# Kernel tuning notes

Measured on AMD Instinct MI355X. Metric: run time of the kernel, lower is better.

Reference implementation:

```python
import jax, jax.numpy as jnp
import numpy as np

NUM_STATES = 8
HIDDEN_DIM = 1024
BATCH = 16384
DT = 0.01
PLANCK = 1.0
EPS_NORM = 1e-8
EPS_LOG = 1e-12


def setup_inputs() -> dict:
    key = jax.random.key(0)
    k1, k2, k3, k4, k5 = jax.random.split(key, 5)
    inv_sqrt_d = 1.0 / np.sqrt(HIDDEN_DIM)
    return {
        "input_state": jax.random.normal(k1, (BATCH, HIDDEN_DIM), dtype=jnp.float32),
        "amplitude_real": jax.random.normal(k2, (NUM_STATES, HIDDEN_DIM), dtype=jnp.float32) * inv_sqrt_d,
        "amplitude_imag": jax.random.normal(k3, (NUM_STATES, HIDDEN_DIM), dtype=jnp.float32) * inv_sqrt_d,
        "hamiltonian": jax.random.normal(k4, (NUM_STATES, NUM_STATES), dtype=jnp.float32) * 0.01,
        "projections": jax.random.normal(k5, (NUM_STATES, HIDDEN_DIM, HIDDEN_DIM), dtype=jnp.float32) * 0.01,
    }


def reference(input_state, amplitude_real, amplitude_imag, hamiltonian, projections):
    # complex amplitudes, normalized per state over hidden dim
    amps = amplitude_real + 1j * amplitude_imag  # [S, D] complex64
    norms = jnp.sum(jnp.abs(amps) ** 2, axis=1, keepdims=True)
    amps = amps / jnp.sqrt(norms + EPS_NORM)

    # unitary Hamiltonian evolution: expm(-i H dt / hbar) on the tiny SxS matrix
    H = (hamiltonian + hamiltonian.T) * 0.5
    U = jax.scipy.linalg.expm((-1j * DT / PLANCK) * H.astype(jnp.complex64))  # [S, S]
    amps = U @ amps  # [S, D]

    # decoherence at time_step=0: factor exp(0)=1, thermal noise scale 0 -> identity

    # superposed output: out[b,e] = sum_s Re(amps[s,e]) * (x @ P_s)[b,e]
    w = jnp.real(amps)  # [S, D]
    proj = jnp.einsum('bd,sde->bse', input_state, projections)  # [B, S, D]
    measured_output = jnp.einsum('bse,se->be', proj, w)  # [B, D]

    # measurement probabilities (computational basis)
    probs = jnp.abs(amps) ** 2
    probs = probs / (probs.sum(axis=0, keepdims=True) + EPS_NORM)
    collapse_prob = probs.mean(axis=1)  # [S]

    # metrics on rank-1 density matrix rho = outer(v, conj(v)), v = amps.flatten():
    # eigenvalues are {||v||^2, 0, ...} so the von Neumann entropy reduces to one term,
    # and sum|rho| = (sum|v|)^2, tr|diag| = sum|v|^2.
    v_abs = jnp.abs(amps.reshape(-1))
    lam = jnp.sum(v_abs ** 2)
    entanglement_entropy = -(lam * jnp.log(lam + EPS_LOG))
    coherence = jnp.sum(v_abs) ** 2 - lam

    amplitude_distribution = jnp.abs(amps) ** 2
    phase_evolution = jnp.angle(amps)

    return (measured_output, collapse_prob, entanglement_entropy, coherence,
            amplitude_distribution, phase_evolution)
```

## Files before the change

### kernel.cpp

```cpp
#include <hip/hip_runtime.h>
#include <hip/hip_bf16.h>

#define NSTATES 8
#define HD      1024
#define NBATCH  16384
#define NT      16

#define OUT_MEAS 0
#define OUT_CP   16777216
#define OUT_ENT  16777224
#define OUT_COH  16777225
#define OUT_AD   16777226
#define OUT_PH   16785418

typedef __attribute__((ext_vector_type(8))) short short8;
typedef __attribute__((ext_vector_type(4))) float f32x4;

__device__ __forceinline__ short f2bf(float f) {
    union { float f; unsigned u; } x; x.f = f;
    unsigned r = x.u + 0x7fffu + ((x.u >> 16) & 1u);
    return (short)(r >> 16);
}

__device__ __forceinline__ unsigned cvtpk(float lo, float hi) {
    unsigned r;
    asm("v_cvt_pk_bf16_f32 %0, %1, %2" : "=v"(r) : "v"(lo), "v"(hi));
    return r;
}

__device__ __forceinline__ short8 pack8pk(float4 a, float4 b) {
    union { unsigned u[4]; short8 s; } r;
    r.u[0] = cvtpk(a.x, a.y);
    r.u[1] = cvtpk(a.z, a.w);
    r.u[2] = cvtpk(b.x, b.y);
    r.u[3] = cvtpk(b.z, b.w);
    return r.s;
}

__global__ __launch_bounds__(1024) void k_amps(const float* __restrict__ AR,
                                               const float* __restrict__ AI,
                                               const float* __restrict__ H,
                                               float* __restrict__ out,
                                               float* __restrict__ w) {
    __shared__ float redA[16 * NSTATES];
    __shared__ float redB[16 * 10];
    __shared__ float norms[NSTATES];
    __shared__ float sA[8][8], sA2[8][8], sA3[8][8];
    __shared__ float Ur[8][8], Ui[8][8];
    __shared__ float lamsa[2];

    const int tid = threadIdx.x;
    const int lane = tid & 63, wid = tid >> 6;
    const int d = tid;

    float arv[NSTATES], aiv[NSTATES];
    #pragma unroll
    for (int s = 0; s < NSTATES; s++) {
        arv[s] = AR[s * HD + d];
        aiv[s] = AI[s * HD + d];
    }
    float p[NSTATES];
    #pragma unroll
    for (int s = 0; s < NSTATES; s++) p[s] = arv[s] * arv[s] + aiv[s] * aiv[s];
    #pragma unroll
    for (int s = 0; s < NSTATES; s++)
        #pragma unroll
        for (int o = 32; o > 0; o >>= 1) p[s] += __shfl_down(p[s], o, 64);
    if (lane == 0)
        #pragma unroll
        for (int s = 0; s < NSTATES; s++) redA[wid * NSTATES + s] = p[s];
    if (tid < 64) {
        int i = tid >> 3, j = tid & 7;
        sA[i][j] = 0.5f * (H[i * 8 + j] + H[j * 8 + i]) * 0.01f;
    }
    __syncthreads();
    if (tid < 8) {
        float acc = 0.f;
        #pragma unroll
        for (int v = 0; v < 16; v++) acc += redA[v * NSTATES + tid];
        norms[tid] = acc;
    }
    if (tid < 64) {
        int i = tid >> 3, j = tid & 7;
        float acc = 0.f;
        #pragma unroll
        for (int k = 0; k < 8; k++) acc += sA[i][k] * sA[k][j];
        sA2[i][j] = acc;
    }
    __syncthreads();
    if (tid < 64) {
        int i = tid >> 3, j = tid & 7;
        float acc = 0.f;
        #pragma unroll
        for (int k = 0; k < 8; k++) acc += sA2[i][k] * sA[k][j];
        sA3[i][j] = acc;
        Ur[i][j] = ((i == j) ? 1.f : 0.f) - 0.5f * sA2[i][j];
        Ui[i][j] = -(sA[i][j] - sA3[i][j] * (1.f / 6.f));
    }
    __syncthreads();

    #pragma unroll
    for (int s = 0; s < NSTATES; s++) {
        float inv = 1.0f / sqrtf(norms[s] + 1e-8f);
        arv[s] *= inv;
        aiv[s] *= inv;
    }
    float nr[NSTATES], ni[NSTATES];
    #pragma unroll
    for (int s = 0; s < NSTATES; s++) {
        float xr = 0.f, xi = 0.f;
        #pragma unroll
        for (int t = 0; t < NSTATES; t++) {
            float ur = Ur[s][t], ui = Ui[s][t];
            xr += ur * arv[t] - ui * aiv[t];
            xi += ur * aiv[t] + ui * arv[t];
        }
        nr[s] = xr; ni[s] = xi;
    }
    float dist[NSTATES], csum = 0.f, sabs = 0.f;
    #pragma unroll
    for (int s = 0; s < NSTATES; s++) {
        dist[s] = nr[s] * nr[s] + ni[s] * ni[s];
        csum += dist[s];
        sabs += sqrtf(dist[s]);
    }
    #pragma unroll
    for (int s = 0; s < NSTATES; s++) {
        out[OUT_AD + s * HD + d] = dist[s];
        out[OUT_PH + s * HD + d] = atan2f(ni[s], nr[s]);
        w[s * HD + d] = nr[s];
    }
    float cinv = 1.0f / (csum + 1e-8f);
    float q[10];
    #pragma unroll
    for (int s = 0; s < NSTATES; s++) q[s] = dist[s] * cinv;
    q[8] = csum; q[9] = sabs;
    #pragma unroll
    for (int v = 0; v < 10; v++)
        #pragma unroll
        for (int o = 32; o > 0; o >>= 1) q[v] += __shfl_down(q[v], o, 64);
    if (lane == 0)
        #pragma unroll
        for (int v = 0; v < 10; v++) redB[wid * 10 + v] = q[v];
    __syncthreads();
    if (tid < 10) {
        float acc = 0.f;
        #pragma unroll
        for (int v = 0; v < 16; v++) acc += redB[v * 10 + tid];
        if (tid < 8)       out[OUT_CP + tid] = acc * (1.0f / HD);
        else               lamsa[tid - 8] = acc;
    }
    __syncthreads();
    if (tid == 0) {
        float lam = lamsa[0], sa = lamsa[1];
        out[OUT_ENT] = -(lam * logf(lam + 1e-12f));
        out[OUT_COH] = sa * sa - lam;
    }
}

__global__ __launch_bounds__(256) void k_project_t(const float* __restrict__ P,
                                                   const float* __restrict__ w,
                                                   short* __restrict__ Mt) {
    __shared__ float tile[64][65];
    int d0 = (blockIdx.x >> 4) * 64;
    int e0 = (blockIdx.x & 15) * 64;
    int tx = threadIdx.x & 63, ty = threadIdx.x >> 6;
    float wv[NSTATES];
    #pragma unroll
    for (int s = 0; s < NSTATES; s++) wv[s] = w[s * HD + e0 + tx];
    #pragma unroll
    for (int j = 0; j < 16; j++) {
        int r = ty + 4 * j;
        float acc = 0.f;
        #pragma unroll
        for (int s = 0; s < NSTATES; s++)
            acc += wv[s] * P[(size_t)s * HD * HD + (size_t)(d0 + r) * HD + e0 + tx];
        tile[r][tx] = acc;
    }
    __syncthreads();
    #pragma unroll
    for (int j = 0; j < 16; j++) {
        int er = ty + 4 * j;
        Mt[(size_t)(e0 + er) * HD + d0 + tx] = f2bf(tile[tx][er]);
    }
}


__device__ __forceinline__ void stage_half_B(const short* __restrict__ srcBase,
                                             int rowbase, int h, int t2,
                                             short* dst, const int* goff,
                                             const int* ldsoff) {
    #pragma unroll
    for (int i = 0; i < 2; i++) {
        const short* g = srcBase + (size_t)(rowbase + h * 128) * HD + t2 * 64 + goff[i];
        __builtin_amdgcn_global_load_lds(
            (const __attribute__((address_space(1))) void*)g,
            (__attribute__((address_space(3))) void*)(dst + h * 8192 + ldsoff[i]),
            16, 0, 0);
    }
}

#define XLOAD(dst, h, t2)                                                      \
    {                                                                          \
        const float* b_ = X + (size_t)(brow + (h) * 128) * HD + (t2) * 64;     \
        dst[0] = *reinterpret_cast<const float4*>(b_ + goff[0]);               \
        dst[1] = *reinterpret_cast<const float4*>(b_ + goff[0] + 4);           \
        dst[2] = *reinterpret_cast<const float4*>(b_ + goff[1]);               \
        dst[3] = *reinterpret_cast<const float4*>(b_ + goff[1] + 4);           \
    }

#define XWRITE(dstlds, src)                                                    \
    {                                                                          \
        *reinterpret_cast<short8*>((dstlds) + ldsoff[0]) = pack8pk(src[0], src[1]); \
        *reinterpret_cast<short8*>((dstlds) + ldsoff[1]) = pack8pk(src[2], src[3]); \
    }

#define LOAD_A(qa)                                                             \
    _Pragma("unroll") for (int mf = 0; mf < 4; mf++)                           \
    _Pragma("unroll") for (int kk = 0; kk < 2; kk++)                           \
        af[mf][kk] = *reinterpret_cast<const short8*>(                         \
            &Acur[((qa) * 128 + wr64 + mf * 16 + ln15) * 64 + kx[kk]]);

#define LOAD_B_TO(dst, qb)                                                     \
    _Pragma("unroll") for (int nf = 0; nf < 2; nf++)                           \
    _Pragma("unroll") for (int kk = 0; kk < 2; kk++)                           \
        dst[nf][kk] = *reinterpret_cast<const short8*>(                        \
            &Bcur[((qb) * 128 + wn32 + nf * 16 + ln15) * 64 + kx[kk]]);

#define MFMA_P(qa, qb, breg)                                                   \
    _Pragma("unroll") for (int mf = 0; mf < 4; mf++)                           \
    _Pragma("unroll") for (int nf = 0; nf < 2; nf++)                           \
    _Pragma("unroll") for (int kk = 0; kk < 2; kk++)                           \
        acc[(qa) * 4 + mf][(qb) * 2 + nf] =                                    \
            __builtin_amdgcn_mfma_f32_16x16x32_bf16(                           \
                af[mf][kk], breg[nf][kk], acc[(qa) * 4 + mf][(qb) * 2 + nf], 0, 0, 0);

#define STORE_Q(qa, qb)                                                        \
    _Pragma("unroll") for (int mf = 0; mf < 4; mf++)                           \
    _Pragma("unroll") for (int nf = 0; nf < 2; nf++)                           \
    _Pragma("unroll") for (int j = 0; j < 4; j++) {                            \
        int r = brow + (qa) * 128 + wr64 + mf * 16 + l16 * 4 + j;              \
        int c = bcol + (qb) * 128 + wn32 + nf * 16 + ln15;                     \
        out[(size_t)r * HD + c] = acc[(qa) * 4 + mf][(qb) * 2 + nf][j];        \
    }

__global__ __launch_bounds__(512, 1) void k_gemm_jit3(const float* __restrict__ X,
                                                      const short* __restrict__ Mt,
                                                      float* __restrict__ out) {
    __shared__ short As[2][256 * 64];
    __shared__ short Bs[2][256 * 64];

    const int bid = blockIdx.x;
    const int swz = (bid & 7) * 32 + (bid >> 3);
    const int brow = (swz >> 2) * 256;
    const int bcol = (swz & 3) * 256;

    const int tid  = threadIdx.x;
    const int lane = tid & 63, wid = tid >> 6;
    const int wr = wid >> 2, wn = wid & 3;
    const int ln15 = lane & 15, l16 = lane >> 4;
    const int wr64 = wr * 64;
    const int wn32 = wn * 32;

    int kx[2];
    kx[0] = ((l16 + 0) ^ (ln15 & 7)) * 8;
    kx[1] = ((l16 + 4) ^ (ln15 & 7)) * 8;

    int goff[2], ldsoff[2];
    #pragma unroll
    for (int i = 0; i < 2; i++) {
        int c = tid + 512 * i;
        int row = c >> 3, kc = c & 7;
        goff[i]   = row * HD + ((kc ^ (row & 7)) * 8);
        ldsoff[i] = c * 8;
    }

    short* A0 = &As[0][0]; short* A1b = &As[1][0];
    short* B0 = &Bs[0][0]; short* B1b = &Bs[1][0];

    f32x4 acc[8][4];
    #pragma unroll
    for (int m = 0; m < 8; m++)
        #pragma unroll
        for (int n = 0; n < 4; n++) acc[m][n] = (f32x4){0.f, 0.f, 0.f, 0.f};

    float4 xrL[4], xrH[4];

    XLOAD(xrL, 0, 0);
    XLOAD(xrH, 1, 0);
    stage_half_B(Mt, bcol, 0, 0, B0, goff, ldsoff);
    stage_half_B(Mt, bcol, 1, 0, B0, goff, ldsoff);
    stage_half_B(Mt, bcol, 1, 1, B1b, goff, ldsoff);
    XWRITE(A0, xrL);
    XWRITE(A0 + 8192, xrH);
    XLOAD(xrL, 0, 1);
    asm volatile("s_waitcnt vmcnt(6) lgkmcnt(0)" ::: "memory");
    __builtin_amdgcn_s_barrier();

    short8 af[4][2], bfL[2][2], bfH[2][2];

    #pragma unroll 1
    for (int t = 0; t < NT - 1; t++) {
        const int cur = t & 1;
        short* Acur  = cur ? A1b : A0;
        short* Bcur  = cur ? B1b : B0;
        short* Anext = cur ? A0 : A1b;
        short* Bnext = cur ? B0 : B1b;

        LOAD_A(0); LOAD_B_TO(bfL, 0);
        if (t + 1 < NT) XLOAD(xrH, 1, (t + 1));
        __builtin_amdgcn_s_barrier();
        __builtin_amdgcn_s_setprio(1);
        MFMA_P(0, 0, bfL);
        __builtin_amdgcn_s_setprio(0);

        LOAD_B_TO(bfH, 1);
        if (t + 1 < NT) stage_half_B(Mt, bcol, 0, t + 1, Bnext, goff, ldsoff);
        __builtin_amdgcn_s_barrier();
        __builtin_amdgcn_s_setprio(1);
        MFMA_P(0, 1, bfH);
        __builtin_amdgcn_s_setprio(0);

        LOAD_A(1);
        if (t + 1 < NT) XWRITE(Anext, xrL);
        __builtin_amdgcn_s_barrier();
        __builtin_amdgcn_s_setprio(1);
        MFMA_P(1, 1, bfH);
        __builtin_amdgcn_s_setprio(0);

        if (t + 1 < NT) XWRITE(Anext + 8192, xrH);
        if (t + 2 < NT) {
            XLOAD(xrL, 0, (t + 2));
            stage_half_B(Mt, bcol, 1, t + 2, Bcur, goff, ldsoff);
        }
        if (t + 2 < NT)      asm volatile("s_waitcnt vmcnt(6) lgkmcnt(0)" ::: "memory");
        else if (t + 1 < NT) asm volatile("s_waitcnt vmcnt(0) lgkmcnt(0)" ::: "memory");
        __builtin_amdgcn_s_barrier();
        __builtin_amdgcn_s_setprio(1);
        MFMA_P(1, 0, bfL);
        __builtin_amdgcn_s_setprio(0);
    }

    {
        short* Acur = A1b;
        short* Bcur = B1b;

        LOAD_A(0); LOAD_B_TO(bfL, 0);
        __builtin_amdgcn_s_setprio(1);
        MFMA_P(0, 0, bfL);
        __builtin_amdgcn_s_setprio(0);
        STORE_Q(0, 0);

        LOAD_B_TO(bfH, 1);
        __builtin_amdgcn_s_setprio(1);
        MFMA_P(0, 1, bfH);
        __builtin_amdgcn_s_setprio(0);
        STORE_Q(0, 1);

        LOAD_A(1);
        __builtin_amdgcn_s_setprio(1);
        MFMA_P(1, 1, bfH);
        __builtin_amdgcn_s_setprio(0);
        STORE_Q(1, 1);

        __builtin_amdgcn_s_setprio(1);
        MFMA_P(1, 0, bfL);
        __builtin_amdgcn_s_setprio(0);
        STORE_Q(1, 0);
    }
}

extern "C" void kernel_launch(void* const* d_in, const int* in_sizes, int n_in,
                              void* d_out, int out_size, void* d_ws, size_t ws_size,
                              hipStream_t stream) {
    const float* X  = (const float*)d_in[0];
    const float* AR = (const float*)d_in[1];
    const float* AI = (const float*)d_in[2];
    const float* H  = (const float*)d_in[3];
    const float* P  = (const float*)d_in[4];
    float* out = (float*)d_out;

    char* ws = (char*)d_ws;
    float* w  = (float*)ws;
    short* Mt = (short*)(ws + 32768);

    k_amps<<<1, 1024, 0, stream>>>(AR, AI, H, out, w);
    k_project_t<<<256, 256, 0, stream>>>(P, w, Mt);
    k_gemm_jit3<<<(NBATCH / 256) * (HD / 256), 512, 0, stream>>>(X, Mt, out);
}
```

Before: 69.21 us.

## Fuse amplitude computation into projection kernel, recomputing norms per block

Merges the single-block amplitude kernel and the projection/transpose kernel into one 257-block launch. Each block recomputes the state norms and the 8x8 unitary itself, then the 256 projection blocks derive their slice of the real weights locally, while one extra block writes the distribution, phase and scalar metrics. This drops one kernel launch and the serial dependency on a one-block kernel, at the cost of every block redundantly reading all amplitude data to compute the norms.

```diff
diff --git a/kernel.cpp b/kernel.cpp
--- a/kernel.cpp
+++ b/kernel.cpp
@@ -37,49 +37,50 @@
     return r.s;
 }
 
-__global__ __launch_bounds__(1024) void k_amps(const float* __restrict__ AR,
-                                               const float* __restrict__ AI,
-                                               const float* __restrict__ H,
-                                               float* __restrict__ out,
-                                               float* __restrict__ w) {
-    __shared__ float redA[16 * NSTATES];
-    __shared__ float redB[16 * 10];
+__global__ __launch_bounds__(256) void k_pre(const float* __restrict__ P,
+                                             const float* __restrict__ AR,
+                                             const float* __restrict__ AI,
+                                             const float* __restrict__ H,
+                                             short* __restrict__ Mt,
+                                             float* __restrict__ out) {
+    __shared__ float redN[4][NSTATES];
     __shared__ float norms[NSTATES];
-    __shared__ float sA[8][8], sA2[8][8], sA3[8][8];
+    __shared__ float sA[8][8], sA2[8][8];
     __shared__ float Ur[8][8], Ui[8][8];
+    __shared__ float tile[64][65];
+    __shared__ float redC[4][10];
     __shared__ float lamsa[2];
 
+    const int bid = blockIdx.x;
     const int tid = threadIdx.x;
     const int lane = tid & 63, wid = tid >> 6;
-    const int d = tid;
-
-    float arv[NSTATES], aiv[NSTATES];
-    #pragma unroll
-    for (int s = 0; s < NSTATES; s++) {
-        arv[s] = AR[s * HD + d];
-        aiv[s] = AI[s * HD + d];
-    }
+
     float p[NSTATES];
     #pragma unroll
-    for (int s = 0; s < NSTATES; s++) p[s] = arv[s] * arv[s] + aiv[s] * aiv[s];
+    for (int s = 0; s < NSTATES; s++) p[s] = 0.f;
+    #pragma unroll
+    for (int c = 0; c < 4; c++) {
+        int d = tid + c * 256;
+        #pragma unroll
+        for (int s = 0; s < NSTATES; s++) {
+            float a = AR[s * HD + d], b = AI[s * HD + d];
+            p[s] += a * a + b * b;
+        }
+    }
     #pragma unroll
     for (int s = 0; s < NSTATES; s++)
         #pragma unroll
         for (int o = 32; o > 0; o >>= 1) p[s] += __shfl_down(p[s], o, 64);
     if (lane == 0)
         #pragma unroll
-        for (int s = 0; s < NSTATES; s++) redA[wid * NSTATES + s] = p[s];
+        for (int s = 0; s < NSTATES; s++) redN[wid][s] = p[s];
     if (tid < 64) {
         int i = tid >> 3, j = tid & 7;
         sA[i][j] = 0.5f * (H[i * 8 + j] + H[j * 8 + i]) * 0.01f;
     }
     __syncthreads();
-    if (tid < 8) {
-        float acc = 0.f;
-        #pragma unroll
-        for (int v = 0; v < 16; v++) acc += redA[v * NSTATES + tid];
-        norms[tid] = acc;
-    }
+    if (tid < 8)
+        norms[tid] = redN[0][tid] + redN[1][tid] + redN[2][tid] + redN[3][tid];
     if (tid < 64) {
         int i = tid >> 3, j = tid & 7;
         float acc = 0.f;
@@ -90,63 +91,105 @@
     __syncthreads();
     if (tid < 64) {
         int i = tid >> 3, j = tid & 7;
-        float acc = 0.f;
-        #pragma unroll
-        for (int k = 0; k < 8; k++) acc += sA2[i][k] * sA[k][j];
-        sA3[i][j] = acc;
+        float a3 = 0.f;
+        #pragma unroll
+        for (int k = 0; k < 8; k++) a3 += sA2[i][k] * sA[k][j];
         Ur[i][j] = ((i == j) ? 1.f : 0.f) - 0.5f * sA2[i][j];
-        Ui[i][j] = -(sA[i][j] - sA3[i][j] * (1.f / 6.f));
+        Ui[i][j] = -(sA[i][j] - a3 * (1.f / 6.f));
     }
     __syncthreads();
 
-    #pragma unroll
-    for (int s = 0; s < NSTATES; s++) {
-        float inv = 1.0f / sqrtf(norms[s] + 1e-8f);
-        arv[s] *= inv;
-        aiv[s] *= inv;
-    }
-    float nr[NSTATES], ni[NSTATES];
-    #pragma unroll
-    for (int s = 0; s < NSTATES; s++) {
-        float xr = 0.f, xi = 0.f;
-        #pragma unroll
-        for (int t = 0; t < NSTATES; t++) {
-            float ur = Ur[s][t], ui = Ui[s][t];
-            xr += ur * arv[t] - ui * aiv[t];
-            xi += ur * aiv[t] + ui * arv[t];
-        }
-        nr[s] = xr; ni[s] = xi;
-    }
-    float dist[NSTATES], csum = 0.f, sabs = 0.f;
-    #pragma unroll
-    for (int s = 0; s < NSTATES; s++) {
-        dist[s] = nr[s] * nr[s] + ni[s] * ni[s];
-        csum += dist[s];
-        sabs += sqrtf(dist[s]);
-    }
-    #pragma unroll
-    for (int s = 0; s < NSTATES; s++) {
-        out[OUT_AD + s * HD + d] = dist[s];
-        out[OUT_PH + s * HD + d] = atan2f(ni[s], nr[s]);
-        w[s * HD + d] = nr[s];
-    }
-    float cinv = 1.0f / (csum + 1e-8f);
+    if (bid < 256) {
+        int d0 = (bid >> 4) * 64;
+        int e0 = (bid & 15) * 64;
+        int tx = tid & 63, ty = tid >> 6;
+        float inv[NSTATES], arv[NSTATES], aiv[NSTATES], wv[NSTATES];
+        #pragma unroll
+        for (int s = 0; s < NSTATES; s++) inv[s] = 1.0f / sqrtf(norms[s] + 1e-8f);
+        #pragma unroll
+        for (int s = 0; s < NSTATES; s++) {
+            arv[s] = AR[s * HD + e0 + tx] * inv[s];
+            aiv[s] = AI[s * HD + e0 + tx] * inv[s];
+        }
+        #pragma unroll
+        for (int s = 0; s < NSTATES; s++) {
+            float xr = 0.f;
+            #pragma unroll
+            for (int t = 0; t < NSTATES; t++)
+                xr += Ur[s][t] * arv[t] - Ui[s][t] * aiv[t];
+            wv[s] = xr;
+        }
+        #pragma unroll
+        for (int j = 0; j < 16; j++) {
+            int r = ty + 4 * j;
+            float acc = 0.f;
+            #pragma unroll
+            for (int s = 0; s < NSTATES; s++)
+                acc += wv[s] * P[(size_t)s * HD * HD + (size_t)(d0 + r) * HD + e0 + tx];
+            tile[r][tx] = acc;
+        }
+        __syncthreads();
+        #pragma unroll
+        for (int j = 0; j < 16; j++) {
+            int er = ty + 4 * j;
+            Mt[(size_t)(e0 + er) * HD + d0 + tx] = f2bf(tile[tx][er]);
+        }
+        return;
+    }
+
+    float inv[NSTATES];
+    #pragma unroll
+    for (int s = 0; s < NSTATES; s++) inv[s] = 1.0f / sqrtf(norms[s] + 1e-8f);
     float q[10];
     #pragma unroll
-    for (int s = 0; s < NSTATES; s++) q[s] = dist[s] * cinv;
-    q[8] = csum; q[9] = sabs;
+    for (int v = 0; v < 10; v++) q[v] = 0.f;
+    #pragma unroll
+    for (int c = 0; c < 4; c++) {
+        int d = tid + c * 256;
+        float arv[NSTATES], aiv[NSTATES], nr[NSTATES], ni[NSTATES];
+        #pragma unroll
+        for (int s = 0; s < NSTATES; s++) {
+            arv[s] = AR[s * HD + d] * inv[s];
+            aiv[s] = AI[s * HD + d] * inv[s];
+        }
+        #pragma unroll
+        for (int s = 0; s < NSTATES; s++) {
+            float xr = 0.f, xi = 0.f;
+            #pragma unroll
+            for (int t = 0; t < NSTATES; t++) {
+                float ur = Ur[s][t], ui = Ui[s][t];
+                xr += ur * arv[t] - ui * aiv[t];
+                xi += ur * aiv[t] + ui * arv[t];
+            }
+            nr[s] = xr; ni[s] = xi;
+        }
+        float dist[NSTATES], csum = 0.f, sabs = 0.f;
+        #pragma unroll
+        for (int s = 0; s < NSTATES; s++) {
+            dist[s] = nr[s] * nr[s] + ni[s] * ni[s];
+            csum += dist[s];
+            sabs += sqrtf(dist[s]);
+        }
+        #pragma unroll
+        for (int s = 0; s < NSTATES; s++) {
+            out[OUT_AD + s * HD + d] = dist[s];
+            out[OUT_PH + s * HD + d] = atan2f(ni[s], nr[s]);
+        }
+        float cinv = 1.0f / (csum + 1e-8f);
+        #pragma unroll
+        for (int s = 0; s < NSTATES; s++) q[s] += dist[s] * cinv;
+        q[8] += csum; q[9] += sabs;
+    }
     #pragma unroll
     for (int v = 0; v < 10; v++)
         #pragma unroll
         for (int o = 32; o > 0; o >>= 1) q[v] += __shfl_down(q[v], o, 64);
     if (lane == 0)
         #pragma unroll
-        for (int v = 0; v < 10; v++) redB[wid * 10 + v] = q[v];
+        for (int v = 0; v < 10; v++) redC[wid][v] = q[v];
     __syncthreads();
     if (tid < 10) {
-        float acc = 0.f;
-        #pragma unroll
-        for (int v = 0; v < 16; v++) acc += redB[v * 10 + tid];
+        float acc = redC[0][tid] + redC[1][tid] + redC[2][tid] + redC[3][tid];
         if (tid < 8)       out[OUT_CP + tid] = acc * (1.0f / HD);
         else               lamsa[tid - 8] = acc;
     }
@@ -155,33 +198,6 @@
         float lam = lamsa[0], sa = lamsa[1];
         out[OUT_ENT] = -(lam * logf(lam + 1e-12f));
         out[OUT_COH] = sa * sa - lam;
-    }
-}
-
-__global__ __launch_bounds__(256) void k_project_t(const float* __restrict__ P,
-                                                   const float* __restrict__ w,
-                                                   short* __restrict__ Mt) {
-    __shared__ float tile[64][65];
-    int d0 = (blockIdx.x >> 4) * 64;
-    int e0 = (blockIdx.x & 15) * 64;
-    int tx = threadIdx.x & 63, ty = threadIdx.x >> 6;
-    float wv[NSTATES];
-    #pragma unroll
-    for (int s = 0; s < NSTATES; s++) wv[s] = w[s * HD + e0 + tx];
-    #pragma unroll
-    for (int j = 0; j < 16; j++) {
-        int r = ty + 4 * j;
-        float acc = 0.f;
-        #pragma unroll
-        for (int s = 0; s < NSTATES; s++)
-            acc += wv[s] * P[(size_t)s * HD * HD + (size_t)(d0 + r) * HD + e0 + tx];
-        tile[r][tx] = acc;
-    }
-    __syncthreads();
-    #pragma unroll
-    for (int j = 0; j < 16; j++) {
-        int er = ty + 4 * j;
-        Mt[(size_t)(e0 + er) * HD + d0 + tx] = f2bf(tile[tx][er]);
     }
 }
 
@@ -381,10 +397,8 @@
     float* out = (float*)d_out;
 
     char* ws = (char*)d_ws;
-    float* w  = (float*)ws;
-    short* Mt = (short*)(ws + 32768);
-
-    k_amps<<<1, 1024, 0, stream>>>(AR, AI, H, out, w);
-    k_project_t<<<256, 256, 0, stream>>>(P, w, Mt);
+    short* Mt = (short*)ws;
+
+    k_pre<<<257, 256, 0, stream>>>(P, AR, AI, H, Mt, out);
     k_gemm_jit3<<<(NBATCH / 256) * (HD / 256), 512, 0, stream>>>(X, Mt, out);
 }
```

Result: slower. 71.15 us (+2.8%).

## Restructure GEMM main loop into two-phase schedule with fewer barriers

Applied to the files above, without the earlier changes.

Replaces the four-phase per-iteration schedule with a two-phase one. All B fragments are read from LDS up front and the next B tile is staged into the alternate buffer in one step, instead of prefetching half of B two tiles ahead. This halves the barriers per K-step and lets each phase issue more MFMAs back to back. The cost is higher register pressure from holding bfL and bfH together, and less interleaving of global loads with compute, which may expose memory latency.

```diff
diff --git a/kernel.cpp b/kernel.cpp
--- a/kernel.cpp
+++ b/kernel.cpp
@@ -244,9 +244,9 @@
         out[(size_t)r * HD + c] = acc[(qa) * 4 + mf][(qb) * 2 + nf][j];        \
     }
 
-__global__ __launch_bounds__(512, 1) void k_gemm_jit3(const float* __restrict__ X,
-                                                      const short* __restrict__ Mt,
-                                                      float* __restrict__ out) {
+__global__ __launch_bounds__(512, 1) void k_gemm_2ph(const float* __restrict__ X,
+                                                     const short* __restrict__ Mt,
+                                                     float* __restrict__ out) {
     __shared__ short As[2][256 * 64];
     __shared__ short Bs[2][256 * 64];
 
@@ -290,11 +290,10 @@
     XLOAD(xrH, 1, 0);
     stage_half_B(Mt, bcol, 0, 0, B0, goff, ldsoff);
     stage_half_B(Mt, bcol, 1, 0, B0, goff, ldsoff);
-    stage_half_B(Mt, bcol, 1, 1, B1b, goff, ldsoff);
     XWRITE(A0, xrL);
     XWRITE(A0 + 8192, xrH);
     XLOAD(xrL, 0, 1);
-    asm volatile("s_waitcnt vmcnt(6) lgkmcnt(0)" ::: "memory");
+    asm volatile("s_waitcnt vmcnt(4) lgkmcnt(0)" ::: "memory");
     __builtin_amdgcn_s_barrier();
 
     short8 af[4][2], bfL[2][2], bfH[2][2];
@@ -307,36 +306,25 @@
         short* Anext = cur ? A0 : A1b;
         short* Bnext = cur ? B0 : B1b;
 
-        LOAD_A(0); LOAD_B_TO(bfL, 0);
-        if (t + 1 < NT) XLOAD(xrH, 1, (t + 1));
+        LOAD_A(0); LOAD_B_TO(bfL, 0); LOAD_B_TO(bfH, 1);
+        XLOAD(xrH, 1, (t + 1));
+        stage_half_B(Mt, bcol, 0, t + 1, Bnext, goff, ldsoff);
+        stage_half_B(Mt, bcol, 1, t + 1, Bnext, goff, ldsoff);
         __builtin_amdgcn_s_barrier();
         __builtin_amdgcn_s_setprio(1);
         MFMA_P(0, 0, bfL);
-        __builtin_amdgcn_s_setprio(0);
-
-        LOAD_B_TO(bfH, 1);
-        if (t + 1 < NT) stage_half_B(Mt, bcol, 0, t + 1, Bnext, goff, ldsoff);
+        MFMA_P(0, 1, bfH);
+        __builtin_amdgcn_s_setprio(0);
+
+        LOAD_A(1);
+        XWRITE(Anext, xrL);
+        XWRITE(Anext + 8192, xrH);
+        if (t + 2 < NT) XLOAD(xrL, 0, (t + 2));
+        if (t + 2 < NT) asm volatile("s_waitcnt vmcnt(4) lgkmcnt(0)" ::: "memory");
+        else            asm volatile("s_waitcnt vmcnt(0) lgkmcnt(0)" ::: "memory");
         __builtin_amdgcn_s_barrier();
         __builtin_amdgcn_s_setprio(1);
-        MFMA_P(0, 1, bfH);
-        __builtin_amdgcn_s_setprio(0);
-
-        LOAD_A(1);
-        if (t + 1 < NT) XWRITE(Anext, xrL);
-        __builtin_amdgcn_s_barrier();
-        __builtin_amdgcn_s_setprio(1);
         MFMA_P(1, 1, bfH);
-        __builtin_amdgcn_s_setprio(0);
-
-        if (t + 1 < NT) XWRITE(Anext + 8192, xrH);
-        if (t + 2 < NT) {
-            XLOAD(xrL, 0, (t + 2));
-            stage_half_B(Mt, bcol, 1, t + 2, Bcur, goff, ldsoff);
-        }
-        if (t + 2 < NT)      asm volatile("s_waitcnt vmcnt(6) lgkmcnt(0)" ::: "memory");
-        else if (t + 1 < NT) asm volatile("s_waitcnt vmcnt(0) lgkmcnt(0)" ::: "memory");
-        __builtin_amdgcn_s_barrier();
-        __builtin_amdgcn_s_setprio(1);
         MFMA_P(1, 0, bfL);
         __builtin_amdgcn_s_setprio(0);
     }
@@ -345,13 +333,12 @@
         short* Acur = A1b;
         short* Bcur = B1b;
 
-        LOAD_A(0); LOAD_B_TO(bfL, 0);
+        LOAD_A(0); LOAD_B_TO(bfL, 0); LOAD_B_TO(bfH, 1);
         __builtin_amdgcn_s_setprio(1);
         MFMA_P(0, 0, bfL);
         __builtin_amdgcn_s_setprio(0);
         STORE_Q(0, 0);
 
-        LOAD_B_TO(bfH, 1);
         __builtin_amdgcn_s_setprio(1);
         MFMA_P(0, 1, bfH);
         __builtin_amdgcn_s_setprio(0);
@@ -386,5 +373,5 @@
 
     k_amps<<<1, 1024, 0, stream>>>(AR, AI, H, out, w);
     k_project_t<<<256, 256, 0, stream>>>(P, w, Mt);
-    k_gemm_jit3<<<(NBATCH / 256) * (HD / 256), 512, 0, stream>>>(X, Mt, out);
-}
+    k_gemm_2ph<<<(NBATCH / 256) * (HD / 256), 512, 0, stream>>>(X, Mt, out);
+}
```

Measured after the change: 64.51 us (median of 2 runs). 6.8% less time.
